# Kernel tuning notes

Measured on AMD Instinct MI355X. Metric: run time of the kernel, lower is better.

Reference implementation:

```python
import jax, jax.numpy as jnp
import numpy as np

# --- model/problem constants (match init_kwargs) ---
B = 1024      # batch
F = 512       # featureSize
H = 1024      # hiddenSize
S = 8         # symmetrySize
BOX = 12      # boxSize
MAXB = 64     # maxBoxes
MAXSY = 64    # maxSyms
MAXS = 16     # max stack depth (pattern uses <= 2)
L = 126


def setup_inputs() -> dict:
    key = jax.random.key(0)
    ks = jax.random.split(key, 9)

    def lin(k, out_d, in_d):
        k1, k2 = jax.random.split(k)
        bound = 1.0 / np.sqrt(in_d)
        W = jax.random.uniform(k1, (out_d, in_d), minval=-bound, maxval=bound, dtype=jnp.float32)
        b = jax.random.uniform(k2, (out_d,), minval=-bound, maxval=bound, dtype=jnp.float32)
        return W, b

    Wd, bd = lin(ks[0], H, F)      # AdjDecoder.decode
    Wl, bl = lin(ks[1], F, H)      # AdjDecoder.left
    Wr, br = lin(ks[2], F, H)      # AdjDecoder.right
    Wsd, bsd = lin(ks[3], H, F)    # SymDecoder.decode
    Wsf, bsf = lin(ks[4], F, H)    # SymDecoder.left
    Wss, bss = lin(ks[5], S, H)    # SymDecoder.right
    Wbox, bbox = lin(ks[6], BOX, F)  # BoxDecoder.decode

    inputStacks = jax.random.normal(ks[7], (B, F), dtype=jnp.float32)

    # Valid stack program, PROCESSING order: [adj, sym, box] * 42.
    # stack depth: 1 ->(1) 2 ->(2) 2 ->(0) 1 ; 42 boxes, 42 syms.
    proc = np.tile(np.array([1, 2, 0], dtype=np.int32), L // 3)
    stored = proc[::-1].copy()  # forward() processes operations in reverse
    operations = jnp.asarray(np.tile(stored[None, None, :], (B, 1, 1)))  # [B,1,L]

    return {"inputStacks": inputStacks, "operations": operations,
            "Wd": Wd, "bd": bd, "Wl": Wl, "bl": bl, "Wr": Wr, "br": br,
            "Wsd": Wsd, "bsd": bsd, "Wsf": Wsf, "bsf": bsf, "Wss": Wss, "bss": bss,
            "Wbox": Wbox, "bbox": bbox}


def _forward(inputStacks, operations, Wd, bd, Wl, bl, Wr, br,
             Wsd, bsd, Wsf, bsf, Wss, bss, Wbox, bbox):
    Bn, Fn = inputStacks.shape
    ops_proc = jnp.flip(operations[:, 0, :], axis=1).T  # [L, B] processing order

    stack = jnp.zeros((Bn, MAXS, Fn), inputStacks.dtype).at[:, 0, :].set(inputStacks)
    sp = jnp.ones((Bn,), jnp.int32)           # stack pointer (size)
    boxbuf = jnp.zeros((Bn, MAXB, Fn), inputStacks.dtype)
    bc = jnp.zeros((Bn,), jnp.int32)
    symbuf = jnp.zeros((Bn, MAXSY, S), inputStacks.dtype)
    sc = jnp.zeros((Bn,), jnp.int32)
    rows = jnp.arange(Bn)

    def step(carry, op):
        stack, sp, boxbuf, bc, symbuf, sc = carry
        top_idx = jnp.clip(sp - 1, 0, MAXS - 1)
        top = stack[rows, top_idx]                      # [B,F]
        # AdjDecoder on every sample (selected by op==1)
        h = jnp.tanh(top @ Wd.T + bd)
        l = jnp.tanh(h @ Wl.T + bl)
        r = jnp.tanh(h @ Wr.T + br)
        # SymDecoder on every sample (selected by op==2)
        hs = jnp.tanh(top @ Wsd.T + bsd)
        f = jnp.tanh(hs @ Wsf.T + bsf)
        s = jnp.tanh(hs @ Wss.T + bss)

        is0 = op == 0
        is1 = op == 1
        is2 = op == 2
        # value replacing the popped top (for op 1 -> left, op 2 -> folded)
        val_top = jnp.where(is1[:, None], l, jnp.where(is2[:, None], f, top))
        pos = jnp.arange(MAXS)[None, :]
        m_top = (pos == top_idx[:, None]) & (~is0)[:, None]
        m_r = (pos == jnp.clip(sp, 0, MAXS - 1)[:, None]) & is1[:, None]
        stack = jnp.where(m_r[..., None], r[:, None, :],
                          jnp.where(m_top[..., None], val_top[:, None, :], stack))
        posb = jnp.arange(MAXB)[None, :]
        mb = (posb == bc[:, None]) & is0[:, None]
        boxbuf = jnp.where(mb[..., None], top[:, None, :], boxbuf)
        poss = jnp.arange(MAXSY)[None, :]
        ms = (poss == sc[:, None]) & is2[:, None]
        symbuf = jnp.where(ms[..., None], s[:, None, :], symbuf)

        sp = sp + jnp.where(is0, -1, jnp.where(is1, 1, 0)).astype(sp.dtype)
        bc = bc + is0.astype(bc.dtype)
        sc = sc + is2.astype(sc.dtype)
        return (stack, sp, boxbuf, bc, symbuf, sc), None

    (stack, sp, boxbuf, bc, symbuf, sc), _ = jax.lax.scan(
        step, (stack, sp, boxbuf, bc, symbuf, sc), ops_proc)

    # boxStacks[i].reverse(); boxDecoder; pad with zeros to maxBoxes
    jb = jnp.arange(MAXB)
    bidx = bc[:, None] - 1 - jb[None, :]          # reversed order
    bvalid = bidx >= 0
    bfeat = jnp.take_along_axis(boxbuf, jnp.clip(bidx, 0, MAXB - 1)[..., None], axis=1)
    boxes = jnp.tanh(bfeat @ Wbox.T + bbox) * bvalid[..., None].astype(bfeat.dtype)

    js = jnp.arange(MAXSY)
    sidx = sc[:, None] - 1 - js[None, :]
    svalid = sidx >= 0
    syms = jnp.take_along_axis(symbuf, jnp.clip(sidx, 0, MAXSY - 1)[..., None], axis=1)
    syms = syms * svalid[..., None].astype(syms.dtype)

    return boxes, syms  # [B, MAXB, BOX], [B, MAXSY, S]


def reference(inputStacks, operations, Wd, bd, Wl, bl, Wr, br,
              Wsd, bsd, Wsf, bsf, Wss, bss, Wbox, bbox):
    return _forward(inputStacks, operations, Wd, bd, Wl, bl, Wr, br,
                    Wsd, bsd, Wsf, bsf, Wss, bss, Wbox, bbox)
```

## Files before the change

kernel.cpp:

```cpp
#include <hip/hip_runtime.h>
#include <stdint.h>

#define B_     1024
#define F_     512
#define H_     1024
#define S_     8
#define BOX_   12
#define MAXB_  64
#define MAXSY_ 64
#define L_     126
#define STK_   3
#define NCYC_  42

typedef unsigned short u16;
typedef unsigned int   u32;
typedef unsigned long long u64;
typedef __attribute__((ext_vector_type(8))) short sh8;
typedef __attribute__((ext_vector_type(4))) int   i4;
typedef __attribute__((ext_vector_type(4))) float f4;

#define MFMA16(a,b,c) __builtin_amdgcn_mfma_f32_16x16x32_bf16((a),(b),(c),0,0,0)

#define XCC_ID_IMM (((32 - 1) << 11) | (0 << 6) | 20)

#define POLL_MAX (1 << 22)

constexpr size_t O_FLAG  = 2048;
constexpr size_t O_GFAIL = 2176;
constexpr size_t O_GXCD  = 2304;
constexpr size_t PL_HF = (size_t)H_ * F_ * 2;
constexpr size_t PL_FH = (size_t)F_ * H_ * 2;
constexpr size_t PL_SS = 16384;
constexpr size_t PL_BX = 16384;
constexpr size_t O_WdHi  = 8192;
constexpr size_t O_WdLo  = O_WdHi  + PL_HF;
constexpr size_t O_WsdHi = O_WdLo  + PL_HF;
constexpr size_t O_WsdLo = O_WsdHi + PL_HF;
constexpr size_t O_WlHi  = O_WsdLo + PL_HF;
constexpr size_t O_WlLo  = O_WlHi  + PL_FH;
constexpr size_t O_WrHi  = O_WlLo  + PL_FH;
constexpr size_t O_WrLo  = O_WrHi  + PL_FH;
constexpr size_t O_WsfHi = O_WrLo  + PL_FH;
constexpr size_t O_WsfLo = O_WsfHi + PL_FH;
constexpr size_t O_WssHi = O_WsfLo + PL_FH;
constexpr size_t O_WssLo = O_WssHi + PL_SS;
constexpr size_t O_WbxHi = O_WssLo + PL_SS;
constexpr size_t O_WbxLo = O_WbxHi + PL_BX;
constexpr size_t SZ_STK  = (size_t)B_ * STK_ * F_ * 2;
constexpr size_t O_SHi   = O_WbxLo + PL_BX;
constexpr size_t O_SLo   = O_SHi   + SZ_STK;
constexpr size_t SZ_H    = (size_t)B_ * H_ * 2;
constexpr size_t O_HAHi  = O_SLo   + SZ_STK;
constexpr size_t O_HALo  = O_HAHi  + SZ_H;
constexpr size_t O_HSHi  = O_HALo  + SZ_H;
constexpr size_t O_HSLo  = O_HSHi  + SZ_H;
constexpr size_t SZ_FB   = (size_t)B_ * 512 * 2;
constexpr size_t O_FB0Hi = O_HSLo  + SZ_H;
constexpr size_t O_FB0Lo = O_FB0Hi + SZ_FB;
constexpr size_t O_FB1Hi = O_FB0Lo + SZ_FB;
constexpr size_t O_FB1Lo = O_FB1Hi + SZ_FB;
constexpr size_t WS_NEED = O_FB1Lo + SZ_FB;

__device__ __forceinline__ float bf2float(u16 h) {
    union { u32 u; float f; } v; v.u = ((u32)h) << 16; return v.f;
}
__device__ __forceinline__ u16 bfhi_of(float f) {
    union { float f; u32 u; } v; v.f = f;
    u32 u = v.u;
    return (u16)((u + 0x7fffu + ((u >> 16) & 1u)) >> 16);
}
__device__ __forceinline__ void split2(float x, u16& hi, u16& lo) {
    hi = bfhi_of(x);
    lo = bfhi_of(x - bf2float(hi));
}

template<bool DC>
__device__ __forceinline__ void cst(u16* p, u16 v) {
    if (DC) asm volatile("global_store_short %0, %1, off sc0 sc1"
                         :: "v"(p), "v"((u32)v) : "memory");
    else    asm volatile("global_store_short %0, %1, off"
                         :: "v"(p), "v"((u32)v) : "memory");
}
__device__ __forceinline__ void vdrain() {
    asm volatile("s_waitcnt vmcnt(0)" ::: "memory");
}

__device__ __forceinline__ void cld8(i4& d0, i4& d1, i4& d2, i4& d3,
                                     i4& d4, i4& d5, i4& d6, i4& d7,
    const u16* p0, const u16* p1, const u16* p2, const u16* p3,
    const u16* p4, const u16* p5, const u16* p6, const u16* p7)
{
    asm volatile(
        "global_load_dwordx4 %0, %8, off sc0\n\t"
        "global_load_dwordx4 %1, %9, off sc0\n\t"
        "global_load_dwordx4 %2, %10, off sc0\n\t"
        "global_load_dwordx4 %3, %11, off sc0\n\t"
        "global_load_dwordx4 %4, %12, off sc0\n\t"
        "global_load_dwordx4 %5, %13, off sc0\n\t"
        "global_load_dwordx4 %6, %14, off sc0\n\t"
        "global_load_dwordx4 %7, %15, off sc0\n\t"
        "s_waitcnt vmcnt(0)"
        : "=&v"(d0),"=&v"(d1),"=&v"(d2),"=&v"(d3),
          "=&v"(d4),"=&v"(d5),"=&v"(d6),"=&v"(d7)
        : "v"(p0),"v"(p1),"v"(p2),"v"(p3),"v"(p4),"v"(p5),"v"(p6),"v"(p7));
}

__device__ void split_range(const float* __restrict__ s, u16* hi, u16* lo,
                            int n, int t0, int stride) {
    for (int i = t0; i < n; i += stride) {
        float v = s[i];
        u16 h = bfhi_of(v);
        hi[i] = h;
        lo[i] = bfhi_of(v - bf2float(h));
    }
}

__global__ void grass_prep(const float* __restrict__ X, const int* __restrict__ ops,
                           const float* __restrict__ Wd, const float* __restrict__ Wl,
                           const float* __restrict__ Wr, const float* __restrict__ Wsd,
                           const float* __restrict__ Wsf, const float* __restrict__ Wss,
                           const float* __restrict__ Wbox, char* __restrict__ ws)
{
    const int t0 = blockIdx.x * blockDim.x + threadIdx.x;
    const int st = gridDim.x * blockDim.x;
    split_range(Wd,  (u16*)(ws + O_WdHi),  (u16*)(ws + O_WdLo),  H_ * F_, t0, st);
    split_range(Wsd, (u16*)(ws + O_WsdHi), (u16*)(ws + O_WsdLo), H_ * F_, t0, st);
    split_range(Wl,  (u16*)(ws + O_WlHi),  (u16*)(ws + O_WlLo),  F_ * H_, t0, st);
    split_range(Wr,  (u16*)(ws + O_WrHi),  (u16*)(ws + O_WrLo),  F_ * H_, t0, st);
    split_range(Wsf, (u16*)(ws + O_WsfHi), (u16*)(ws + O_WsfLo), F_ * H_, t0, st);
    split_range(Wss, (u16*)(ws + O_WssHi), (u16*)(ws + O_WssLo), S_ * H_, t0, st);
    split_range(Wbox,(u16*)(ws + O_WbxHi), (u16*)(ws + O_WbxLo), BOX_ * F_, t0, st);
    u16* SHi = (u16*)(ws + O_SHi);
    u16* SLo = (u16*)(ws + O_SLo);
    for (int i = t0; i < B_ * F_; i += st) {
        int e = i >> 9, k = i & (F_ - 1);
        float v = X[i];
        u16 h = bfhi_of(v);
        size_t off = (size_t)e * STK_ * F_ + k;
        SHi[off] = h;
        SLo[off] = bfhi_of(v - bf2float(h));
    }
    int* flag = (int*)(ws + O_FLAG);
    for (int i = t0; i < B_ * L_; i += st) {
        int t = i % L_;
        int tm = t % 3;
        int expect = (tm == 0) ? 0 : ((tm == 1) ? 2 : 1);
        if (ops[i] != expect) {
            __hip_atomic_store(flag, 1, __ATOMIC_RELAXED, __HIP_MEMORY_SCOPE_AGENT);
            break;
        }
    }
}

__device__ __forceinline__ void gbar(int* bar, int target) {
    vdrain();
    __syncthreads();
    if (threadIdx.x == 0) {
        __hip_atomic_fetch_add(bar, 1, __ATOMIC_RELAXED, __HIP_MEMORY_SCOPE_AGENT);
        while (__hip_atomic_load(bar, __ATOMIC_RELAXED, __HIP_MEMORY_SCOPE_AGENT) < target)
            __builtin_amdgcn_s_sleep(2);
    }
    __syncthreads();
}
__device__ __forceinline__ void gbarT(int* bar, int target) {
    vdrain();
    __syncthreads();
    if (threadIdx.x == 0) {
        __hip_atomic_fetch_add(bar, 1, __ATOMIC_RELAXED, __HIP_MEMORY_SCOPE_AGENT);
        for (int it = 0; it < POLL_MAX; ++it) {
            if (__hip_atomic_load(bar, __ATOMIC_RELAXED, __HIP_MEMORY_SCOPE_AGENT) >= target) break;
            __builtin_amdgcn_s_sleep(2);
        }
    }
    __syncthreads();
}
__device__ __forceinline__ void gwaitT(int* ctr, int target) {
    if (threadIdx.x == 0) {
        for (int it = 0; it < POLL_MAX; ++it) {
            if (__hip_atomic_load(ctr, __ATOMIC_RELAXED, __HIP_MEMORY_SCOPE_AGENT) >= target) break;
            __builtin_amdgcn_s_sleep(2);
        }
    }
    __syncthreads();
}

__device__ __forceinline__ void stage256(u16* __restrict__ lds,
    const u16* __restrict__ AHi, const u16* __restrict__ ALo,
    const int* __restrict__ aOff, int kbase, int tid)
{
    const int wv = tid >> 6, lane = tid & 63;
    const int rsub = lane >> 5;
    const int c8 = (lane & 31) * 8;
    int off[8];
#pragma unroll
    for (int i = 0; i < 8; ++i) off[i] = aOff[i * 8 + wv * 2 + rsub] + kbase + c8;
    const int sw = ((wv * 2 + rsub) & 7) << 3;
    i4 d0,d1,d2,d3,d4,d5,d6,d7;
    cld8(d0,d1,d2,d3,d4,d5,d6,d7,
         AHi+off[0], AHi+off[1], AHi+off[2], AHi+off[3],
         AHi+off[4], AHi+off[5], AHi+off[6], AHi+off[7]);
#define STO(ii, dv, base) { const int m = (ii) * 8 + wv * 2 + rsub; \
                            *(i4*)((base) + m * 256 + (c8 ^ sw)) = dv; }
    STO(0,d0,lds) STO(1,d1,lds) STO(2,d2,lds) STO(3,d3,lds)
    STO(4,d4,lds) STO(5,d5,lds) STO(6,d6,lds) STO(7,d7,lds)
    cld8(d0,d1,d2,d3,d4,d5,d6,d7,
         ALo+off[0], ALo+off[1], ALo+off[2], ALo+off[3],
         ALo+off[4], ALo+off[5], ALo+off[6], ALo+off[7]);
    u16* ldsLo = lds + 64 * 256;
    STO(0,d0,ldsLo) STO(1,d1,ldsLo) STO(2,d2,ldsLo) STO(3,d3,ldsLo)
    STO(4,d4,ldsLo) STO(5,d5,ldsLo) STO(6,d6,ldsLo) STO(7,d7,ldsLo)
#undef STO
}

__device__ __forceinline__ void stageA_dc(u16* __restrict__ lds,
    const u16* __restrict__ AHi, const u16* __restrict__ ALo,
    const int* __restrict__ aOff, int kbase, int tid)
{
    const int wv = tid >> 6, lane = tid & 63;
    const int kk = kbase + lane * 8;
    int off[16];
#pragma unroll
    for (int i = 0; i < 16; ++i) off[i] = aOff[i * 4 + wv] + kk;
    u64 v[64];
#pragma unroll
    for (int i = 0; i < 16; ++i) {
        const u64* s = (const u64*)(AHi + off[i]);
        v[2 * i]     = __hip_atomic_load(s,     __ATOMIC_RELAXED, __HIP_MEMORY_SCOPE_AGENT);
        v[2 * i + 1] = __hip_atomic_load(s + 1, __ATOMIC_RELAXED, __HIP_MEMORY_SCOPE_AGENT);
    }
#pragma unroll
    for (int i = 0; i < 16; ++i) {
        const u64* s = (const u64*)(ALo + off[i]);
        v[32 + 2 * i] = __hip_atomic_load(s,     __ATOMIC_RELAXED, __HIP_MEMORY_SCOPE_AGENT);
        v[33 + 2 * i] = __hip_atomic_load(s + 1, __ATOMIC_RELAXED, __HIP_MEMORY_SCOPE_AGENT);
    }
#pragma unroll
    for (int i = 0; i < 16; ++i) {
        const int m = i * 4 + wv;
        u16* d = lds + m * 512 + ((lane * 8) ^ ((m & 7) << 3));
        ((u64*)d)[0] = v[2 * i];
        ((u64*)d)[1] = v[2 * i + 1];
        u64* d2 = (u64*)(d + 32768);
        d2[0] = v[32 + 2 * i];
        d2[1] = v[33 + 2 * i];
    }
}

template<int CW>
__device__ __forceinline__ void kloop64(const u16* __restrict__ lds,
    const u16* __restrict__ WHi, const u16* __restrict__ WLo,
    int nRow0, int Kw, int kofs, f4 c[2][2], int lane, int wv4)
{
    const int quad = lane >> 4, mr = lane & 15;
    const int mh = wv4 & 1, nh = (wv4 >> 1) & 1;
    const int m0 = (mh * 2) * 16 + mr, m1 = m0 + 16;
    const int n0 = nRow0 + (nh * 2) * 16 + mr, n1 = n0 + 16;
    const u16* b0h = WHi + (size_t)n0 * Kw + kofs;
    const u16* b1h = WHi + (size_t)n1 * Kw + kofs;
    const u16* b0l = WLo + (size_t)n0 * Kw + kofs;
    const u16* b1l = WLo + (size_t)n1 * Kw + kofs;
    const int sw = (m0 & 7) << 3;
    const u16* A0h = lds + m0 * CW;
    const u16* A1h = lds + m1 * CW;
#pragma unroll 2
    for (int kb = 0; kb < CW; kb += 64) {
        const int k0 = kb + quad * 8, k1 = k0 + 32;
        const int x0 = k0 ^ sw, x1 = k1 ^ sw;
        sh8 B0H0 = *(const sh8*)(b0h + k0), B1H0 = *(const sh8*)(b1h + k0);
        sh8 B0L0 = *(const sh8*)(b0l + k0), B1L0 = *(const sh8*)(b1l + k0);
        sh8 B0H1 = *(const sh8*)(b0h + k1), B1H1 = *(const sh8*)(b1h + k1);
        sh8 B0L1 = *(const sh8*)(b0l + k1), B1L1 = *(const sh8*)(b1l + k1);
        sh8 A0H0 = *(const sh8*)(A0h + x0);
        sh8 A1H0 = *(const sh8*)(A1h + x0);
        sh8 A0L0 = *(const sh8*)(A0h + 64 * CW + x0);
        sh8 A1L0 = *(const sh8*)(A1h + 64 * CW + x0);
        sh8 A0H1 = *(const sh8*)(A0h + x1);
        sh8 A1H1 = *(const sh8*)(A1h + x1);
        sh8 A0L1 = *(const sh8*)(A0h + 64 * CW + x1);
        sh8 A1L1 = *(const sh8*)(A1h + 64 * CW + x1);
        c[0][0]=MFMA16(A0H0,B0H0,c[0][0]); c[0][1]=MFMA16(A0H0,B1H0,c[0][1]);
        c[1][0]=MFMA16(A1H0,B0H0,c[1][0]); c[1][1]=MFMA16(A1H0,B1H0,c[1][1]);
        c[0][0]=MFMA16(A0H0,B0L0,c[0][0]); c[0][1]=MFMA16(A0H0,B1L0,c[0][1]);
        c[1][0]=MFMA16(A1H0,B0L0,c[1][0]); c[1][1]=MFMA16(A1H0,B1L0,c[1][1]);
        c[0][0]=MFMA16(A0L0,B0H0,c[0][0]); c[0][1]=MFMA16(A0L0,B1H0,c[0][1]);
        c[1][0]=MFMA16(A1L0,B0H0,c[1][0]); c[1][1]=MFMA16(A1L0,B1H0,c[1][1]);
        c[0][0]=MFMA16(A0H1,B0H1,c[0][0]); c[0][1]=MFMA16(A0H1,B1H1,c[0][1]);
        c[1][0]=MFMA16(A1H1,B0H1,c[1][0]); c[1][1]=MFMA16(A1H1,B1H1,c[1][1]);
        c[0][0]=MFMA16(A0H1,B0L1,c[0][0]); c[0][1]=MFMA16(A0H1,B1L1,c[0][1]);
        c[1][0]=MFMA16(A1H1,B0L1,c[1][0]); c[1][1]=MFMA16(A1H1,B1L1,c[1][1]);
        c[0][0]=MFMA16(A0L1,B0H1,c[0][0]); c[0][1]=MFMA16(A0L1,B1H1,c[0][1]);
        c[1][0]=MFMA16(A1L1,B0H1,c[1][0]); c[1][1]=MFMA16(A1L1,B1H1,c[1][1]);
    }
}

template<int CW>
__device__ __forceinline__ void kloop16(const u16* __restrict__ lds,
    const u16* __restrict__ WHi, const u16* __restrict__ WLo,
    int nValid, int Kw, int kofs, f4& c, int lane, int wv)
{
    const int quad = lane >> 4, mr = lane & 15;
    const int m = wv * 16 + mr;
    const int sm = (m & 7) << 3;
    const u16* Am = lds + m * CW;
    const bool nb = (mr < nValid);
    const u16* bh = WHi + (size_t)mr * Kw + kofs;
    const u16* bl = WLo + (size_t)mr * Kw + kofs;
#pragma unroll 2
    for (int kb = 0; kb < CW; kb += 64) {
        const int k0 = kb + quad * 8, k1 = k0 + 32;
        const int x0 = k0 ^ sm, x1 = k1 ^ sm;
        sh8 bH0 = {0,0,0,0,0,0,0,0}, bL0 = {0,0,0,0,0,0,0,0};
        sh8 bH1 = {0,0,0,0,0,0,0,0}, bL1 = {0,0,0,0,0,0,0,0};
        if (nb) {
            bH0 = *(const sh8*)(bh + k0); bL0 = *(const sh8*)(bl + k0);
            bH1 = *(const sh8*)(bh + k1); bL1 = *(const sh8*)(bl + k1);
        }
        sh8 aH0 = *(const sh8*)(Am + x0);
        sh8 aL0 = *(const sh8*)(Am + 64 * CW + x0);
        sh8 aH1 = *(const sh8*)(Am + x1);
        sh8 aL1 = *(const sh8*)(Am + 64 * CW + x1);
        c = MFMA16(aH0, bH0, c);
        c = MFMA16(aH0, bL0, c);
        c = MFMA16(aL0, bH0, c);
        c = MFMA16(aH1, bH1, c);
        c = MFMA16(aH1, bL1, c);
        c = MFMA16(aL1, bH1, c);
    }
}

__device__ __forceinline__ void zacc(f4 c[2][2]) {
    f4 z = {0.f, 0.f, 0.f, 0.f};
    c[0][0] = z; c[0][1] = z; c[1][0] = z; c[1][1] = z;
}

__device__ __forceinline__ void gemmK(u16* __restrict__ Ab,
    const u16* __restrict__ AHi, const u16* __restrict__ ALo, const int* __restrict__ aOff,
    const u16* __restrict__ WHi, const u16* __restrict__ WLo, int nRow0, int Kw,
    f4 c[2][2], int tid, int lane, int wv)
{
    zacc(c);
    for (int h = 0; h < Kw; h += 512) {
        __syncthreads();
        stageA_dc(Ab, AHi, ALo, aOff, h, tid);
        __syncthreads();
        kloop64<512>(Ab, WHi, WLo, nRow0, Kw, h, c, lane, wv);
    }
}
__device__ __forceinline__ void gemmK16(u16* __restrict__ Ab,
    const u16* __restrict__ AHi, const u16* __restrict__ ALo, const int* __restrict__ aOff,
    const u16* __restrict__ WHi, const u16* __restrict__ WLo, int nValid, int Kw,
    f4& c, int tid, int lane, int wv)
{
    f4 z = {0.f, 0.f, 0.f, 0.f};
    c = z;
    for (int h = 0; h < Kw; h += 512) {
        __syncthreads();
        stageA_dc(Ab, AHi, ALo, aOff, h, tid);
        __syncthreads();
        kloop16<512>(Ab, WHi, WLo, nValid, Kw, h, c, lane, wv);
    }
}

__device__ __forceinline__ void pipe_gemm64(u16* __restrict__ Ab,
    const u16* __restrict__ AHi, const u16* __restrict__ ALo, const int* __restrict__ aOff,
    const u16* __restrict__ WHi, const u16* __restrict__ WLo, int col0, int Kw,
    f4 c[2][2], int tid, int lane, int wv)
{
    zacc(c);
    for (int h = 0; h < Kw; h += 256) {
        __syncthreads();
        stage256(Ab, AHi, ALo, aOff, h, tid);
        __syncthreads();
        kloop64<256>(Ab, WHi, WLo, col0, Kw, h, c, lane, wv);
    }
}

template<bool DC>
__device__ __forceinline__ void ep_h(const f4 c[2][2], const float* __restrict__ bias,
                                     int colBase, int e0, u16* DHi, u16* DLo,
                                     int lane, int wv4)
{
    const int quad = lane >> 4, mr = lane & 15;
    const int mh = wv4 & 1, nh = (wv4 >> 1) & 1;
#pragma unroll
    for (int mi = 0; mi < 2; ++mi)
#pragma unroll
    for (int ni = 0; ni < 2; ++ni)
#pragma unroll
    for (int r = 0; r < 4; ++r) {
        int mm = (mh * 2 + mi) * 16 + quad * 4 + r;
        int nn = (nh * 2 + ni) * 16 + mr;
        float v = tanhf(c[mi][ni][r] + bias[colBase + nn]);
        u16 hi, lo; split2(v, hi, lo);
        size_t off = (size_t)(e0 + mm) * H_ + colBase + nn;
        cst<DC>(DHi + off, hi);
        cst<DC>(DLo + off, lo);
    }
}

template<bool DC>
__device__ __forceinline__ void ep_slot(const f4 c[2][2], const float* __restrict__ bias,
                                        int colBase, int slot, int e0,
                                        u16* SHi, u16* SLo, int lane, int wv4)
{
    const int quad = lane >> 4, mr = lane & 15;
    const int mh = wv4 & 1, nh = (wv4 >> 1) & 1;
#pragma unroll
    for (int mi = 0; mi < 2; ++mi)
#pragma unroll
    for (int ni = 0; ni < 2; ++ni)
#pragma unroll
    for (int r = 0; r < 4; ++r) {
        int mm = (mh * 2 + mi) * 16 + quad * 4 + r;
        int nn = (nh * 2 + ni) * 16 + mr;
        float v = tanhf(c[mi][ni][r] + bias[colBase + nn]);
        u16 hi, lo; split2(v, hi, lo);
        size_t off = ((size_t)(e0 + mm) * STK_ + slot) * F_ + colBase + nn;
        cst<DC>(SHi + off, hi);
        cst<DC>(SLo + off, lo);
    }
}

template<bool DC>
__device__ __forceinline__ void ep_fb(const f4 c[2][2], const float* __restrict__ bias,
                                      int colBase, int e0, u16* FHi, u16* FLo,
                                      int lane, int wv4)
{
    const int quad = lane >> 4, mr = lane & 15;
    const int mh = wv4 & 1, nh = (wv4 >> 1) & 1;
#pragma unroll
    for (int mi = 0; mi < 2; ++mi)
#pragma unroll
    for (int ni = 0; ni < 2; ++ni)
#pragma unroll
    for (int r = 0; r < 4; ++r) {
        int mm = (mh * 2 + mi) * 16 + quad * 4 + r;
        int nn = (nh * 2 + ni) * 16 + mr;
        float v = tanhf(c[mi][ni][r] + bias[colBase + nn]);
        u16 hi, lo; split2(v, hi, lo);
        size_t off = (size_t)(e0 + mm) * 512 + colBase + nn;
        cst<DC>(FHi + off, hi);
        cst<DC>(FLo + off, lo);
    }
}

template<bool DC>
__device__ __forceinline__ void ep_stack(const f4 c[2][2], const float* __restrict__ bias,
                                         int colBase, int opSel, bool useRi, int tix, int e0,
                                         const unsigned char* opsL, const int* spA,
                                         u16* SHi, u16* SLo, int lane, int wv)
{
    const int quad = lane >> 4, mr = lane & 15;
    const int mh = wv & 1, nh = (wv >> 1) & 1;
#pragma unroll
    for (int mi = 0; mi < 2; ++mi)
#pragma unroll
    for (int ni = 0; ni < 2; ++ni)
#pragma unroll
    for (int r = 0; r < 4; ++r) {
        int mm = (mh * 2 + mi) * 16 + quad * 4 + r;
        int nn = (nh * 2 + ni) * 16 + mr;
        if (opsL[mm * L_ + tix] != opSel) continue;
        int sp = spA[mm];
        int slot = useRi ? sp : sp - 1;
        slot = slot < 0 ? 0 : (slot > STK_ - 1 ? STK_ - 1 : slot);
        float v = tanhf(c[mi][ni][r] + bias[colBase + nn]);
        u16 hi, lo; split2(v, hi, lo);
        size_t off = ((size_t)(e0 + mm) * STK_ + slot) * F_ + colBase + nn;
        cst<DC>(SHi + off, hi);
        cst<DC>(SLo + off, lo);
    }
}

__device__ __forceinline__ void ep_small(const f4& c, const float* __restrict__ bias,
                                         int nValid, int opSel, int tix, int e0,
                                         const unsigned char* opsL, const int* eCnt, const int* eTot,
                                         float* __restrict__ outBase, int rowStride, int ncols,
                                         int lane, int wv)
{
    const int nn = lane & 15;
    if (nn >= nValid) return;
#pragma unroll
    for (int r = 0; r < 4; ++r) {
        int mm = wv * 16 + (lane >> 4) * 4 + r;
        if (opsL[mm * L_ + tix] != opSel) continue;
        int slot = eTot[mm] - 1 - eCnt[mm];
        if (slot < 0 || slot >= 64) continue;
        float v = tanhf(c[r] + bias[nn]);
        outBase[(size_t)(e0 + mm) * rowStride + slot * ncols + nn] = v;
    }
}

__device__ __forceinline__ void ep_small_u(const f4& c, const float* __restrict__ bias,
                                           int nValid, int slot, int e0,
                                           float* __restrict__ outBase, int rowStride, int ncols,
                                           int lane, int wv)
{
    const int nn = lane & 15;
    if (nn >= nValid) return;
#pragma unroll
    for (int r = 0; r < 4; ++r) {
        int mm = wv * 16 + (lane >> 4) * 4 + r;
        outBase[(size_t)(e0 + mm) * rowStride + slot * ncols + nn] = tanhf(c[r] + bias[nn]);
    }
}

__global__ __launch_bounds__(256, 2) void grass_pipe(
    const float* __restrict__ bd, const float* __restrict__ bl, const float* __restrict__ br,
    const float* __restrict__ bsd, const float* __restrict__ bsf, const float* __restrict__ bss,
    const float* __restrict__ bbox,
    char* __restrict__ ws, float* __restrict__ out)
{
    if (__hip_atomic_load((int*)(ws + O_FLAG), __ATOMIC_RELAXED, __HIP_MEMORY_SCOPE_AGENT))
        return;

    const int tid  = threadIdx.x;
    const int lane = tid & 63, wv = tid >> 6;
    const int j    = blockIdx.x >> 4;
    const int gid  = blockIdx.x & 15;
    const int e0   = gid * 64;

    const u16* WdHi  = (const u16*)(ws + O_WdHi);
    const u16* WdLo  = (const u16*)(ws + O_WdLo);
    const u16* WsdHi = (const u16*)(ws + O_WsdHi);
    const u16* WsdLo = (const u16*)(ws + O_WsdLo);
    const u16* WlHi  = (const u16*)(ws + O_WlHi);
    const u16* WlLo  = (const u16*)(ws + O_WlLo);
    const u16* WrHi  = (const u16*)(ws + O_WrHi);
    const u16* WrLo  = (const u16*)(ws + O_WrLo);
    const u16* WsfHi = (const u16*)(ws + O_WsfHi);
    const u16* WsfLo = (const u16*)(ws + O_WsfLo);
    const u16* WssHi = (const u16*)(ws + O_WssHi);
    const u16* WssLo = (const u16*)(ws + O_WssLo);
    const u16* WbxHi = (const u16*)(ws + O_WbxHi);
    const u16* WbxLo = (const u16*)(ws + O_WbxLo);
    u16* SHi  = (u16*)(ws + O_SHi);
    u16* SLo  = (u16*)(ws + O_SLo);
    u16* HAHi = (u16*)(ws + O_HAHi);
    u16* HALo = (u16*)(ws + O_HALo);
    u16* HSHi = (u16*)(ws + O_HSHi);
    u16* HSLo = (u16*)(ws + O_HSLo);
    u16* FB0Hi = (u16*)(ws + O_FB0Hi);
    u16* FB0Lo = (u16*)(ws + O_FB0Lo);
    u16* FB1Hi = (u16*)(ws + O_FB1Hi);
    u16* FB1Lo = (u16*)(ws + O_FB1Lo);
    int* cbar = (int*)ws + gid * 32;
    int* sbar = cbar + 1;
    int* pbar = cbar + 3;
    int* gx   = (int*)(ws + O_GXCD) + gid * 32;
    int* gf   = (int*)(ws + O_GFAIL) + gid;

    float* outB = out;
    float* outS = out + (size_t)B_ * MAXB_ * BOX_;

    __shared__ __align__(16) u16 Abuf[2 * 64 * 256];
    __shared__ int aS0[64], aR1[64], aR2[64], aHH[64], aFB[64];

    if (tid < 64) {
        aS0[tid] = ((e0 + tid) * STK_ + 0) * F_;
        aR1[tid] = ((e0 + tid) * STK_ + 1) * F_;
        aR2[tid] = ((e0 + tid) * STK_ + 2) * F_;
        aHH[tid] = (e0 + tid) * H_;
        aFB[tid] = (e0 + tid) * 512;
    }

    const int myxcd = (int)(__builtin_amdgcn_s_getreg(XCC_ID_IMM) & 0xf);
    if (tid == 0)
        __hip_atomic_store(gx + j, myxcd, __ATOMIC_RELAXED, __HIP_MEMORY_SCOPE_AGENT);
    gbarT(pbar, 32);
    if (tid < 32) {
        int ox = __hip_atomic_load(gx + tid, __ATOMIC_RELAXED, __HIP_MEMORY_SCOPE_AGENT);
        if (ox != myxcd)
            __hip_atomic_store(gf, 1, __ATOMIC_RELAXED, __HIP_MEMORY_SCOPE_AGENT);
    }
    gbarT(pbar, 64);
    if (__hip_atomic_load(gf, __ATOMIC_RELAXED, __HIP_MEMORY_SCOPE_AGENT))
        return;

    f4 cA[2][2];
    f4 cs;

    if (j < 16) {
        for (int cyc = 0; cyc < NCYC_; ++cyc) {
            pipe_gemm64(Abuf, SHi, SLo, aS0, WdHi, WdLo, j * 64, F_, cA, tid, lane, wv);
            ep_h<false>(cA, bd, j * 64, e0, HAHi, HALo, lane, wv);
            gbarT(cbar, 16 * (2 * cyc + 1));
            if (j < 8) {
                pipe_gemm64(Abuf, HAHi, HALo, aHH, WlHi, WlLo, j * 64, H_, cA, tid, lane, wv);
                ep_slot<false>(cA, bl, j * 64, 0, e0, SHi, SLo, lane, wv);
            } else {
                const int rs = 1 + (cyc & 1);
                pipe_gemm64(Abuf, HAHi, HALo, aHH, WrHi, WrLo, (j - 8) * 64, H_, cA, tid, lane, wv);
                if (cyc >= 2) gwaitT(sbar, 16 * (2 * (cyc - 2) + 1));
                ep_slot<false>(cA, br, (j - 8) * 64, rs, e0, SHi, SLo, lane, wv);
            }
            gbarT(cbar, 16 * (2 * cyc + 2));
        }
    } else {
        const int role = j - 16;
        for (int cyc = 0; cyc < NCYC_; ++cyc) {
            gwaitT(cbar, 16 * (2 * cyc + 2));
            const int* aR = (cyc & 1) ? aR2 : aR1;
            pipe_gemm64(Abuf, SHi, SLo, aR, WsdHi, WsdLo, role * 64, F_, cA, tid, lane, wv);
            ep_h<false>(cA, bsd, role * 64, e0, HSHi, HSLo, lane, wv);
            gbarT(sbar, 16 * (2 * cyc + 1));
            if (role < 8) {
                u16* FH = (cyc & 1) ? FB1Hi : FB0Hi;
                u16* FL = (cyc & 1) ? FB1Lo : FB0Lo;
                pipe_gemm64(Abuf, HSHi, HSLo, aHH, WsfHi, WsfLo, role * 64, H_, cA, tid, lane, wv);
                ep_fb<false>(cA, bsf, role * 64, e0, FH, FL, lane, wv);
            } else if (role == 8) {
                f4 z = {0.f, 0.f, 0.f, 0.f}; cs = z;
                for (int h = 0; h < H_; h += 256) {
                    __syncthreads();
                    stage256(Abuf, HSHi, HSLo, aHH, h, tid);
                    __syncthreads();
                    kloop16<256>(Abuf, WssHi, WssLo, S_, H_, h, cs, lane, wv);
                }
                ep_small_u(cs, bss, S_, NCYC_ - 1 - cyc, e0, outS, MAXSY_ * S_, S_, lane, wv);
            } else if (role == 9 && cyc >= 1) {
                const u16* FH = ((cyc - 1) & 1) ? FB1Hi : FB0Hi;
                const u16* FL = ((cyc - 1) & 1) ? FB1Lo : FB0Lo;
                f4 z = {0.f, 0.f, 0.f, 0.f}; cs = z;
                for (int h = 0; h < 512; h += 256) {
                    __syncthreads();
                    stage256(Abuf, FH, FL, aFB, h, tid);
                    __syncthreads();
                    kloop16<256>(Abuf, WbxHi, WbxLo, BOX_, 512, h, cs, lane, wv);
                }
                ep_small_u(cs, bbox, BOX_, NCYC_ - (cyc - 1) - 1, e0, outB, MAXB_ * BOX_, BOX_, lane, wv);
            }
            gbarT(sbar, 16 * (2 * cyc + 2));
        }
        if (role == 9) {
            const u16* FH = ((NCYC_ - 1) & 1) ? FB1Hi : FB0Hi;
            const u16* FL = ((NCYC_ - 1) & 1) ? FB1Lo : FB0Lo;
            f4 z = {0.f, 0.f, 0.f, 0.f}; cs = z;
            for (int h = 0; h < 512; h += 256) {
                __syncthreads();
                stage256(Abuf, FH, FL, aFB, h, tid);
                __syncthreads();
                kloop16<256>(Abuf, WbxHi, WbxLo, BOX_, 512, h, cs, lane, wv);
            }
            ep_small_u(cs, bbox, BOX_, 0, e0, outB, MAXB_ * BOX_, BOX_, lane, wv);
        }
    }
}

__global__ __launch_bounds__(256, 2) void grass_legacy(
    const int* __restrict__ ops,
    const float* __restrict__ bd, const float* __restrict__ bl, const float* __restrict__ br,
    const float* __restrict__ bsd, const float* __restrict__ bsf, const float* __restrict__ bss,
    const float* __restrict__ bbox,
    char* __restrict__ ws, float* __restrict__ out)
{
    const int tid  = threadIdx.x;
    const int lane = tid & 63, wv = tid >> 6;
    const int gid  = blockIdx.x >> 4;
    const int j    = blockIdx.x & 15;
    const int e0   = gid * 64;

    {
        int nonuni = __hip_atomic_load((int*)(ws + O_FLAG), __ATOMIC_RELAXED, __HIP_MEMORY_SCOPE_AGENT);
        int gfl = __hip_atomic_load((int*)(ws + O_GFAIL) + gid, __ATOMIC_RELAXED, __HIP_MEMORY_SCOPE_AGENT);
        if (!nonuni && !gfl) return;
    }

    const u16* WdHi  = (const u16*)(ws + O_WdHi);
    const u16* WdLo  = (const u16*)(ws + O_WdLo);
    const u16* WsdHi = (const u16*)(ws + O_WsdHi);
    const u16* WsdLo = (const u16*)(ws + O_WsdLo);
    const u16* WlHi  = (const u16*)(ws + O_WlHi);
    const u16* WlLo  = (const u16*)(ws + O_WlLo);
    const u16* WrHi  = (const u16*)(ws + O_WrHi);
    const u16* WrLo  = (const u16*)(ws + O_WrLo);
    const u16* WsfHi = (const u16*)(ws + O_WsfHi);
    const u16* WsfLo = (const u16*)(ws + O_WsfLo);
    const u16* WssHi = (const u16*)(ws + O_WssHi);
    const u16* WssLo = (const u16*)(ws + O_WssLo);
    const u16* WbxHi = (const u16*)(ws + O_WbxHi);
    const u16* WbxLo = (const u16*)(ws + O_WbxLo);
    u16* SHi  = (u16*)(ws + O_SHi);
    u16* SLo  = (u16*)(ws + O_SLo);
    u16* HAHi = (u16*)(ws + O_HAHi);
    u16* HALo = (u16*)(ws + O_HALo);
    u16* HSHi = (u16*)(ws + O_HSHi);
    u16* HSLo = (u16*)(ws + O_HSLo);
    int* bar = (int*)ws + gid * 32 + 2;

    float* outB = out;
    float* outS = out + (size_t)B_ * MAXB_ * BOX_;

    __shared__ __align__(16) u16 Abuf[2 * 64 * 512];
    __shared__ unsigned char opsL[64 * L_];
    __shared__ int spA[64], beA[64], seA[64], beF[64], seF[64];
    __shared__ int aStk[64], aHH[64];
    __shared__ int sInfo[2];

    for (int idx = tid; idx < 64 * L_; idx += 256) {
        int e = idx / L_, t = idx - e * L_;
        opsL[idx] = (unsigned char)ops[(size_t)(e0 + e) * L_ + t];
    }
    __syncthreads();
    if (tid < 64) {
        spA[tid] = 1; beA[tid] = 0; seA[tid] = 0;
        int cb = 0, cs2 = 0;
        for (int t = 0; t < L_; ++t) {
            int o = opsL[tid * L_ + t];
            cb += (o == 0); cs2 += (o == 2);
        }
        beF[tid] = cb; seF[tid] = cs2;
        aHH[tid]  = (e0 + tid) * H_;
        aStk[tid] = ((e0 + tid) * STK_ + 0) * F_;
    }
    __syncthreads();

    int epoch = 0;
    f4 c[2][2];
    f4 cs;

    for (int step = 0; step < L_; ++step) {
        const int tix = L_ - 1 - step;
        if (wv == 0) {
            int o  = opsL[lane * L_ + tix];
            int sp = spA[lane];
            unsigned long long bo = __ballot(o  == opsL[0 * L_ + tix]);
            unsigned long long bs = __ballot(sp == spA[0]);
            if (lane == 0) {
                sInfo[0] = o;
                sInfo[1] = (bo == ~0ull && bs == ~0ull) ? 1 : 0;
            }
        }
        __syncthreads();
        const int opU = sInfo[0], uni = sInfo[1];

        if (uni) {
            if (opU == 1) {
                gemmK(Abuf, SHi, SLo, aStk, WdHi, WdLo, j * 64, F_, c, tid, lane, wv);
                ep_h<true>(c, bd, j * 64, e0, HAHi, HALo, lane, wv);
                ++epoch; gbar(bar, 16 * epoch);
                {
                    const u16* W2H = (j < 8) ? WlHi : WrHi;
                    const u16* W2L = (j < 8) ? WlLo : WrLo;
                    const float* b2 = (j < 8) ? bl : br;
                    gemmK(Abuf, HAHi, HALo, aHH, W2H, W2L, (j & 7) * 64, H_, c, tid, lane, wv);
                    ep_stack<true>(c, b2, (j & 7) * 64, 1, j >= 8, tix, e0, opsL, spA, SHi, SLo, lane, wv);
                }
                ++epoch; gbar(bar, 16 * epoch);
            } else if (opU == 2) {
                gemmK(Abuf, SHi, SLo, aStk, WsdHi, WsdLo, j * 64, F_, c, tid, lane, wv);
                ep_h<true>(c, bsd, j * 64, e0, HAHi, HALo, lane, wv);
                ++epoch; gbar(bar, 16 * epoch);
                if (j < 8) {
                    gemmK(Abuf, HAHi, HALo, aHH, WsfHi, WsfLo, j * 64, H_, c, tid, lane, wv);
                    ep_stack<true>(c, bsf, j * 64, 2, false, tix, e0, opsL, spA, SHi, SLo, lane, wv);
                } else if (j == 8) {
                    gemmK16(Abuf, HAHi, HALo, aHH, WssHi, WssLo, S_, H_, cs, tid, lane, wv);
                    ep_small(cs, bss, S_, 2, tix, e0, opsL, seA, seF, outS, MAXSY_ * S_, S_, lane, wv);
                }
                ++epoch; gbar(bar, 16 * epoch);
            } else {
                if (j == 0) {
                    gemmK16(Abuf, SHi, SLo, aStk, WbxHi, WbxLo, BOX_, F_, cs, tid, lane, wv);
                    ep_small(cs, bbox, BOX_, 0, tix, e0, opsL, beA, beF, outB, MAXB_ * BOX_, BOX_, lane, wv);
                }
            }
        } else {
            gemmK(Abuf, SHi, SLo, aStk, WdHi, WdLo, j * 64, F_, c, tid, lane, wv);
            ep_h<true>(c, bd, j * 64, e0, HAHi, HALo, lane, wv);
            gemmK(Abuf, SHi, SLo, aStk, WsdHi, WsdLo, j * 64, F_, c, tid, lane, wv);
            ep_h<true>(c, bsd, j * 64, e0, HSHi, HSLo, lane, wv);
            if (j == 0) {
                gemmK16(Abuf, SHi, SLo, aStk, WbxHi, WbxLo, BOX_, F_, cs, tid, lane, wv);
                ep_small(cs, bbox, BOX_, 0, tix, e0, opsL, beA, beF, outB, MAXB_ * BOX_, BOX_, lane, wv);
            }
            ++epoch; gbar(bar, 16 * epoch);
            if (j < 8) {
                gemmK(Abuf, HAHi, HALo, aHH, WlHi, WlLo, j * 64, H_, c, tid, lane, wv);
                ep_stack<true>(c, bl, j * 64, 1, false, tix, e0, opsL, spA, SHi, SLo, lane, wv);
                gemmK(Abuf, HSHi, HSLo, aHH, WsfHi, WsfLo, j * 64, H_, c, tid, lane, wv);
                ep_stack<true>(c, bsf, j * 64, 2, false, tix, e0, opsL, spA, SHi, SLo, lane, wv);
            } else {
                gemmK(Abuf, HAHi, HALo, aHH, WrHi, WrLo, (j - 8) * 64, H_, c, tid, lane, wv);
                ep_stack<true>(c, br, (j & 7) * 64, 1, true, tix, e0, opsL, spA, SHi, SLo, lane, wv);
                if (j == 8) {
                    gemmK16(Abuf, HSHi, HSLo, aHH, WssHi, WssLo, S_, H_, cs, tid, lane, wv);
                    ep_small(cs, bss, S_, 2, tix, e0, opsL, seA, seF, outS, MAXSY_ * S_, S_, lane, wv);
// ... 34 lines not shown
        v=p2[i]; s2+=w0.x*v.x; s2+=w0.y*v.y; s2+=w0.z*v.z; s2+=w0.w*v.w;
        v=p2[i+1]; t2+=w1.x*v.x; t2+=w1.y*v.y; t2+=w1.z*v.z; t2+=w1.w*v.w;
        v=p3[i]; s3+=w0.x*v.x; s3+=w0.y*v.y; s3+=w0.z*v.z; s3+=w0.w*v.w;
        v=p3[i+1]; t3+=w1.x*v.x; t3+=w1.y*v.y; t3+=w1.z*v.z; t3+=w1.w*v.w;
    }
    r0=s0+t0; r1=s1+t1; r2=s2+t2; r3=s3+t3;
}
__device__ __forceinline__ float fdot1(const float* __restrict__ row,
                                       const float* __restrict__ x, int K4)
{
    const float4* r = (const float4*)row; const float4* p = (const float4*)x;
    float s=0.f,t=0.f;
    for (int i = 0; i < K4; i += 2) {
        float4 w0=r[i], v0=p[i], w1=r[i+1], v1=p[i+1];
        s+=w0.x*v0.x; s+=w0.y*v0.y; s+=w0.z*v0.z; s+=w0.w*v0.w;
        t+=w1.x*v1.x; t+=w1.y*v1.y; t+=w1.z*v1.z; t+=w1.w*v1.w;
    }
    return s+t;
}
#define FB_G 4
__global__ __launch_bounds__(1024) void grass_fallback(
    const float* __restrict__ inputStacks, const int* __restrict__ ops,
    const float* __restrict__ Wd, const float* __restrict__ bd,
    const float* __restrict__ Wl, const float* __restrict__ bl,
    const float* __restrict__ Wr, const float* __restrict__ br,
    const float* __restrict__ Wsd, const float* __restrict__ bsd,
    const float* __restrict__ Wsf, const float* __restrict__ bsf,
    const float* __restrict__ Wss, const float* __restrict__ bss,
    const float* __restrict__ Wbox, const float* __restrict__ bbox,
    float* __restrict__ out)
{
    __shared__ float stk[FB_G][STK_][F_];
    __shared__ float hh[FB_G][H_];
    __shared__ float boxtmp[FB_G][MAXB_][BOX_];
    __shared__ float symtmp[FB_G][MAXSY_][S_];
    const int t = threadIdx.x, b0 = blockIdx.x * FB_G;
    for (int idx = t; idx < FB_G*F_; idx += 1024) {
        int g = idx >> 9, k = idx & (F_-1);
        stk[g][0][k] = inputStacks[(size_t)(b0+g)*F_ + k];
    }
    for (int idx = t; idx < FB_G*H_; idx += 1024) hh[idx>>10][idx&(H_-1)] = 0.f;
    int sp[FB_G], bc[FB_G], sc[FB_G];
#pragma unroll
    for (int g = 0; g < FB_G; ++g) { sp[g]=1; bc[g]=0; sc[g]=0; }
    __syncthreads();
    for (int step = 0; step < L_; ++step) {
        int op[FB_G], ti[FB_G], ri[FB_G]; bool a1=false,a2=false,a0=false;
#pragma unroll
        for (int g = 0; g < FB_G; ++g) {
            op[g] = ops[(size_t)(b0+g)*L_ + (L_-1-step)];
            int tt = sp[g]-1; tt = tt<0?0:(tt>STK_-1?STK_-1:tt); ti[g]=tt;
            int rr = sp[g]; ri[g] = rr>STK_-1?STK_-1:rr;
            a1 |= (op[g]==1); a2 |= (op[g]==2); a0 |= (op[g]==0);
        }
        const float *x0=stk[0][ti[0]], *x1=stk[1][ti[1]], *x2=stk[2][ti[2]], *x3=stk[3][ti[3]];
        if (a1) {
            float r0,r1,r2,r3; fdot4(Wd+(size_t)t*F_, x0,x1,x2,x3, F_/4, r0,r1,r2,r3);
            float bb = bd[t];
            if (op[0]==1) hh[0][t]=tanhf(r0+bb); if (op[1]==1) hh[1][t]=tanhf(r1+bb);
            if (op[2]==1) hh[2][t]=tanhf(r2+bb); if (op[3]==1) hh[3][t]=tanhf(r3+bb);
        }
        if (a2) {
            float r0,r1,r2,r3; fdot4(Wsd+(size_t)t*F_, x0,x1,x2,x3, F_/4, r0,r1,r2,r3);
            float bb = bsd[t];
            if (op[0]==2) hh[0][t]=tanhf(r0+bb); if (op[1]==2) hh[1][t]=tanhf(r1+bb);
            if (op[2]==2) hh[2][t]=tanhf(r2+bb); if (op[3]==2) hh[3][t]=tanhf(r3+bb);
        }
        if (a0 && t < FB_G*BOX_) {
            int g = t / BOX_, cc = t - g*BOX_;
            if (op[g]==0) {
                float acc = fdot1(Wbox+(size_t)cc*F_, stk[g][ti[g]], F_/4);
                boxtmp[g][bc[g]][cc] = tanhf(acc + bbox[cc]);
            }
        }
        __syncthreads();
        if (a1) {
            if (t < F_) {
                float r0,r1,r2,r3; fdot4(Wl+(size_t)t*H_, hh[0],hh[1],hh[2],hh[3], H_/4, r0,r1,r2,r3);
                float bb = bl[t];
                if (op[0]==1) stk[0][ti[0]][t]=tanhf(r0+bb); if (op[1]==1) stk[1][ti[1]][t]=tanhf(r1+bb);
                if (op[2]==1) stk[2][ti[2]][t]=tanhf(r2+bb); if (op[3]==1) stk[3][ti[3]][t]=tanhf(r3+bb);
            } else {
                int m = t - F_;
                float r0,r1,r2,r3; fdot4(Wr+(size_t)m*H_, hh[0],hh[1],hh[2],hh[3], H_/4, r0,r1,r2,r3);
                float bb = br[m];
                if (op[0]==1) stk[0][ri[0]][m]=tanhf(r0+bb); if (op[1]==1) stk[1][ri[1]][m]=tanhf(r1+bb);
                if (op[2]==1) stk[2][ri[2]][m]=tanhf(r2+bb); if (op[3]==1) stk[3][ri[3]][m]=tanhf(r3+bb);
            }
        }
        if (a2) {
            if (t < F_) {
                float r0,r1,r2,r3; fdot4(Wsf+(size_t)t*H_, hh[0],hh[1],hh[2],hh[3], H_/4, r0,r1,r2,r3);
                float bb = bsf[t];
                if (op[0]==2) stk[0][ti[0]][t]=tanhf(r0+bb); if (op[1]==2) stk[1][ti[1]][t]=tanhf(r1+bb);
                if (op[2]==2) stk[2][ti[2]][t]=tanhf(r2+bb); if (op[3]==2) stk[3][ti[3]][t]=tanhf(r3+bb);
            } else if (t < F_ + FB_G*S_) {
                int idx = t - F_, g = idx >> 3, cc = idx & 7;
                if (op[g]==2) {
                    float acc = fdot1(Wss+(size_t)cc*H_, hh[g], H_/4);
                    symtmp[g][sc[g]][cc] = tanhf(acc + bss[cc]);
                }
            }
        }
        __syncthreads();
#pragma unroll
        for (int g = 0; g < FB_G; ++g) {
            if (op[g]==1) sp[g]++;
            else if (op[g]==2) sc[g]++;
            else { bc[g]++; sp[g]--; }
        }
    }
#pragma unroll
    for (int g = 0; g < FB_G; ++g) {
        int b = b0 + g;
        float* ob = out + (size_t)b * MAXB_ * BOX_;
        for (int idx = t; idx < MAXB_*BOX_; idx += 1024) {
            int jj = idx / BOX_, cc = idx - jj*BOX_;
            int e = bc[g] - 1 - jj;
            ob[idx] = (e >= 0) ? boxtmp[g][e][cc] : 0.f;
        }
        float* os = out + (size_t)B_*MAXB_*BOX_ + (size_t)b * MAXSY_ * S_;
        for (int idx = t; idx < MAXSY_*S_; idx += 1024) {
            int jj = idx >> 3, cc = idx & 7;
            int e = sc[g] - 1 - jj;
            os[idx] = (e >= 0) ? symtmp[g][e][cc] : 0.f;
        }
    }
}

extern "C" void kernel_launch(void* const* d_in, const int* in_sizes, int n_in,
                              void* d_out, int out_size, void* d_ws, size_t ws_size,
                              hipStream_t stream) {
    (void)in_sizes; (void)n_in;
    const float* X    = (const float*)d_in[0];
    const int*   ops  = (const int*)d_in[1];
    const float* Wd   = (const float*)d_in[2];  const float* bd   = (const float*)d_in[3];
    const float* Wl   = (const float*)d_in[4];  const float* bl   = (const float*)d_in[5];
    const float* Wr   = (const float*)d_in[6];  const float* br   = (const float*)d_in[7];
    const float* Wsd  = (const float*)d_in[8];  const float* bsd  = (const float*)d_in[9];
    const float* Wsf  = (const float*)d_in[10]; const float* bsf  = (const float*)d_in[11];
    const float* Wss  = (const float*)d_in[12]; const float* bss  = (const float*)d_in[13];
    const float* Wbox = (const float*)d_in[14]; const float* bbox = (const float*)d_in[15];
    float* out = (float*)d_out;

    if (ws_size < WS_NEED) {
        grass_fallback<<<dim3(B_/FB_G), dim3(1024), 0, stream>>>(
            X, ops, Wd, bd, Wl, bl, Wr, br, Wsd, bsd, Wsf, bsf, Wss, bss, Wbox, bbox, out);
        return;
    }
    char* ws = (char*)d_ws;
    hipMemsetAsync(d_out, 0, (size_t)out_size * sizeof(float), stream);
    hipMemsetAsync(ws, 0, 8192, stream);
    grass_prep<<<dim3(512), dim3(256), 0, stream>>>(X, ops, Wd, Wl, Wr, Wsd, Wsf, Wss, Wbox, ws);
    grass_pipe<<<dim3(512), dim3(256), 0, stream>>>(bd, bl, br, bsd, bsf, bss, bbox, ws, out);
    grass_legacy<<<dim3(256), dim3(256), 0, stream>>>(ops, bd, bl, br, bsd, bsf, bss, bbox, ws, out);
}
```

Baseline: 2.670 ms.

## Widen pipe GEMM tiles to 128 columns with register-prefetched A staging

Each block in the pipelined kernel now computes 128 output columns instead of 64, so the A tile staged in LDS is reused for two column halves. The grid halves to 256 blocks, with role counts and barrier targets rescaled. Global loads for the next K chunk are issued into registers before the MFMA loop and written to LDS afterward, overlapping load latency with compute. The trade-off is fewer blocks per XCD group, higher register pressure (launch bounds reduced to 1), and longer per-block serial work.

Result: slower. 2.877 ms (+7.8%).

```diff
diff --git a/kernel.cpp b/kernel.cpp
--- a/kernel.cpp
+++ b/kernel.cpp
@@ -105,6 +105,25 @@
         : "v"(p0),"v"(p1),"v"(p2),"v"(p3),"v"(p4),"v"(p5),"v"(p6),"v"(p7));
 }
 
+__device__ __forceinline__ void cld8i(i4& d0, i4& d1, i4& d2, i4& d3,
+                                      i4& d4, i4& d5, i4& d6, i4& d7,
+    const u16* p0, const u16* p1, const u16* p2, const u16* p3,
+    const u16* p4, const u16* p5, const u16* p6, const u16* p7)
+{
+    asm volatile(
+        "global_load_dwordx4 %0, %8, off sc0\n\t"
+        "global_load_dwordx4 %1, %9, off sc0\n\t"
+        "global_load_dwordx4 %2, %10, off sc0\n\t"
+        "global_load_dwordx4 %3, %11, off sc0\n\t"
+        "global_load_dwordx4 %4, %12, off sc0\n\t"
+        "global_load_dwordx4 %5, %13, off sc0\n\t"
+        "global_load_dwordx4 %6, %14, off sc0\n\t"
+        "global_load_dwordx4 %7, %15, off sc0"
+        : "=&v"(d0),"=&v"(d1),"=&v"(d2),"=&v"(d3),
+          "=&v"(d4),"=&v"(d5),"=&v"(d6),"=&v"(d7)
+        : "v"(p0),"v"(p1),"v"(p2),"v"(p3),"v"(p4),"v"(p5),"v"(p6),"v"(p7));
+}
+
 __device__ void split_range(const float* __restrict__ s, u16* hi, u16* lo,
                             int n, int t0, int stride) {
     for (int i = t0; i < n; i += stride) {
@@ -182,6 +201,45 @@
         }
     }
     __syncthreads();
+}
+
+__device__ __forceinline__ void stage_issue(
+    i4& a0, i4& a1, i4& a2, i4& a3, i4& a4, i4& a5, i4& a6, i4& a7,
+    i4& b0, i4& b1, i4& b2, i4& b3, i4& b4, i4& b5, i4& b6, i4& b7,
+    const u16* __restrict__ AHi, const u16* __restrict__ ALo,
+    const int* __restrict__ aOff, int kbase, int tid)
+{
+    const int wv = tid >> 6, lane = tid & 63;
+    const int rsub = lane >> 5;
+    const int c8 = (lane & 31) * 8;
+    int off[8];
+#pragma unroll
+    for (int i = 0; i < 8; ++i) off[i] = aOff[i * 8 + wv * 2 + rsub] + kbase + c8;
+    cld8i(a0,a1,a2,a3,a4,a5,a6,a7,
+          AHi+off[0], AHi+off[1], AHi+off[2], AHi+off[3],
+          AHi+off[4], AHi+off[5], AHi+off[6], AHi+off[7]);
+    cld8i(b0,b1,b2,b3,b4,b5,b6,b7,
+          ALo+off[0], ALo+off[1], ALo+off[2], ALo+off[3],
+          ALo+off[4], ALo+off[5], ALo+off[6], ALo+off[7]);
+}
+__device__ __forceinline__ void stage_write(
+    i4 a0, i4 a1, i4 a2, i4 a3, i4 a4, i4 a5, i4 a6, i4 a7,
+    i4 b0, i4 b1, i4 b2, i4 b3, i4 b4, i4 b5, i4 b6, i4 b7,
+    u16* __restrict__ lds, int tid)
+{
+    vdrain();
+    const int wv = tid >> 6, lane = tid & 63;
+    const int rsub = lane >> 5;
+    const int c8 = (lane & 31) * 8;
+    const int sw = ((wv * 2 + rsub) & 7) << 3;
+    u16* ldsLo = lds + 64 * 256;
+#define STO(ii, dv, base) { const int m = (ii) * 8 + wv * 2 + rsub; \
+                            *(i4*)((base) + m * 256 + (c8 ^ sw)) = dv; }
+    STO(0,a0,lds) STO(1,a1,lds) STO(2,a2,lds) STO(3,a3,lds)
+    STO(4,a4,lds) STO(5,a5,lds) STO(6,a6,lds) STO(7,a7,lds)
+    STO(0,b0,ldsLo) STO(1,b1,ldsLo) STO(2,b2,ldsLo) STO(3,b3,ldsLo)
+    STO(4,b4,ldsLo) STO(5,b5,ldsLo) STO(6,b6,ldsLo) STO(7,b7,ldsLo)
+#undef STO
 }
 
 __device__ __forceinline__ void stage256(u16* __restrict__ lds,
@@ -361,17 +419,30 @@
     }
 }
 
-__device__ __forceinline__ void pipe_gemm64(u16* __restrict__ Ab,
+__device__ __forceinline__ void pipe_gemm128(u16* __restrict__ Ab,
     const u16* __restrict__ AHi, const u16* __restrict__ ALo, const int* __restrict__ aOff,
     const u16* __restrict__ WHi, const u16* __restrict__ WLo, int col0, int Kw,
-    f4 c[2][2], int tid, int lane, int wv)
-{
-    zacc(c);
+    f4 cA[2][2], f4 cB[2][2], int tid, int lane, int wv)
+{
+    zacc(cA); zacc(cB);
+    i4 s0,s1,s2,s3,s4,s5,s6,s7,s8,s9,s10,s11,s12,s13,s14,s15;
+    stage_issue(s0,s1,s2,s3,s4,s5,s6,s7,s8,s9,s10,s11,s12,s13,s14,s15,
+                AHi, ALo, aOff, 0, tid);
+    __syncthreads();
+    stage_write(s0,s1,s2,s3,s4,s5,s6,s7,s8,s9,s10,s11,s12,s13,s14,s15, Ab, tid);
+    __syncthreads();
     for (int h = 0; h < Kw; h += 256) {
-        __syncthreads();
-        stage256(Ab, AHi, ALo, aOff, h, tid);
-        __syncthreads();
-        kloop64<256>(Ab, WHi, WLo, col0, Kw, h, c, lane, wv);
+        const bool more = (h + 256 < Kw);
+        if (more)
+            stage_issue(s0,s1,s2,s3,s4,s5,s6,s7,s8,s9,s10,s11,s12,s13,s14,s15,
+                        AHi, ALo, aOff, h + 256, tid);
+        kloop64<256>(Ab, WHi, WLo, col0,      Kw, h, cA, lane, wv);
+        kloop64<256>(Ab, WHi, WLo, col0 + 64, Kw, h, cB, lane, wv);
+        if (more) {
+            __syncthreads();
+            stage_write(s0,s1,s2,s3,s4,s5,s6,s7,s8,s9,s10,s11,s12,s13,s14,s15, Ab, tid);
+            __syncthreads();
+        }
     }
 }
 
@@ -505,7 +576,7 @@
     }
 }
 
-__global__ __launch_bounds__(256, 2) void grass_pipe(
+__global__ __launch_bounds__(256, 1) void grass_pipe(
     const float* __restrict__ bd, const float* __restrict__ bl, const float* __restrict__ br,
     const float* __restrict__ bsd, const float* __restrict__ bsf, const float* __restrict__ bss,
     const float* __restrict__ bbox,
@@ -567,49 +638,54 @@
     const int myxcd = (int)(__builtin_amdgcn_s_getreg(XCC_ID_IMM) & 0xf);
     if (tid == 0)
         __hip_atomic_store(gx + j, myxcd, __ATOMIC_RELAXED, __HIP_MEMORY_SCOPE_AGENT);
-    gbarT(pbar, 32);
-    if (tid < 32) {
+    gbarT(pbar, 16);
+    if (tid < 16) {
         int ox = __hip_atomic_load(gx + tid, __ATOMIC_RELAXED, __HIP_MEMORY_SCOPE_AGENT);
         if (ox != myxcd)
             __hip_atomic_store(gf, 1, __ATOMIC_RELAXED, __HIP_MEMORY_SCOPE_AGENT);
     }
-    gbarT(pbar, 64);
+    gbarT(pbar, 32);
     if (__hip_atomic_load(gf, __ATOMIC_RELAXED, __HIP_MEMORY_SCOPE_AGENT))
         return;
 
-    f4 cA[2][2];
+    f4 cA[2][2], cB[2][2];
     f4 cs;
 
-    if (j < 16) {
+    if (j < 8) {
         for (int cyc = 0; cyc < NCYC_; ++cyc) {
-            pipe_gemm64(Abuf, SHi, SLo, aS0, WdHi, WdLo, j * 64, F_, cA, tid, lane, wv);
-            ep_h<false>(cA, bd, j * 64, e0, HAHi, HALo, lane, wv);
-            gbarT(cbar, 16 * (2 * cyc + 1));
-            if (j < 8) {
-                pipe_gemm64(Abuf, HAHi, HALo, aHH, WlHi, WlLo, j * 64, H_, cA, tid, lane, wv);
-                ep_slot<false>(cA, bl, j * 64, 0, e0, SHi, SLo, lane, wv);
+            pipe_gemm128(Abuf, SHi, SLo, aS0, WdHi, WdLo, j * 128, F_, cA, cB, tid, lane, wv);
+            ep_h<false>(cA, bd, j * 128,      e0, HAHi, HALo, lane, wv);
+            ep_h<false>(cB, bd, j * 128 + 64, e0, HAHi, HALo, lane, wv);
+            gbarT(cbar, 8 * (2 * cyc + 1));
+            if (j < 4) {
+                pipe_gemm128(Abuf, HAHi, HALo, aHH, WlHi, WlLo, j * 128, H_, cA, cB, tid, lane, wv);
+                ep_slot<false>(cA, bl, j * 128,      0, e0, SHi, SLo, lane, wv);
+                ep_slot<false>(cB, bl, j * 128 + 64, 0, e0, SHi, SLo, lane, wv);
             } else {
                 const int rs = 1 + (cyc & 1);
-                pipe_gemm64(Abuf, HAHi, HALo, aHH, WrHi, WrLo, (j - 8) * 64, H_, cA, tid, lane, wv);
-                if (cyc >= 2) gwaitT(sbar, 16 * (2 * (cyc - 2) + 1));
-                ep_slot<false>(cA, br, (j - 8) * 64, rs, e0, SHi, SLo, lane, wv);
+                pipe_gemm128(Abuf, HAHi, HALo, aHH, WrHi, WrLo, (j - 4) * 128, H_, cA, cB, tid, lane, wv);
+                if (cyc >= 2) gwaitT(sbar, 8 * (2 * (cyc - 2) + 1));
+                ep_slot<false>(cA, br, (j - 4) * 128,      rs, e0, SHi, SLo, lane, wv);
+                ep_slot<false>(cB, br, (j - 4) * 128 + 64, rs, e0, SHi, SLo, lane, wv);
             }
-            gbarT(cbar, 16 * (2 * cyc + 2));
+            gbarT(cbar, 8 * (2 * cyc + 2));
         }
     } else {
-        const int role = j - 16;
+        const int role = j - 8;
         for (int cyc = 0; cyc < NCYC_; ++cyc) {
-            gwaitT(cbar, 16 * (2 * cyc + 2));
+            gwaitT(cbar, 8 * (2 * cyc + 2));
             const int* aR = (cyc & 1) ? aR2 : aR1;
-            pipe_gemm64(Abuf, SHi, SLo, aR, WsdHi, WsdLo, role * 64, F_, cA, tid, lane, wv);
-            ep_h<false>(cA, bsd, role * 64, e0, HSHi, HSLo, lane, wv);
-            gbarT(sbar, 16 * (2 * cyc + 1));
-            if (role < 8) {
+            pipe_gemm128(Abuf, SHi, SLo, aR, WsdHi, WsdLo, role * 128, F_, cA, cB, tid, lane, wv);
+            ep_h<false>(cA, bsd, role * 128,      e0, HSHi, HSLo, lane, wv);
+            ep_h<false>(cB, bsd, role * 128 + 64, e0, HSHi, HSLo, lane, wv);
+            gbarT(sbar, 8 * (2 * cyc + 1));
+            if (role < 4) {
                 u16* FH = (cyc & 1) ? FB1Hi : FB0Hi;
                 u16* FL = (cyc & 1) ? FB1Lo : FB0Lo;
-                pipe_gemm64(Abuf, HSHi, HSLo, aHH, WsfHi, WsfLo, role * 64, H_, cA, tid, lane, wv);
-                ep_fb<false>(cA, bsf, role * 64, e0, FH, FL, lane, wv);
-            } else if (role == 8) {
+                pipe_gemm128(Abuf, HSHi, HSLo, aHH, WsfHi, WsfLo, role * 128, H_, cA, cB, tid, lane, wv);
+                ep_fb<false>(cA, bsf, role * 128,      e0, FH, FL, lane, wv);
+                ep_fb<false>(cB, bsf, role * 128 + 64, e0, FH, FL, lane, wv);
+            } else if (role == 4) {
                 f4 z = {0.f, 0.f, 0.f, 0.f}; cs = z;
                 for (int h = 0; h < H_; h += 256) {
                     __syncthreads();
@@ -618,7 +694,7 @@
                     kloop16<256>(Abuf, WssHi, WssLo, S_, H_, h, cs, lane, wv);
                 }
                 ep_small_u(cs, bss, S_, NCYC_ - 1 - cyc, e0, outS, MAXSY_ * S_, S_, lane, wv);
-            } else if (role == 9 && cyc >= 1) {
+            } else if (role == 5 && cyc >= 1) {
                 const u16* FH = ((cyc - 1) & 1) ? FB1Hi : FB0Hi;
                 const u16* FL = ((cyc - 1) & 1) ? FB1Lo : FB0Lo;
                 f4 z = {0.f, 0.f, 0.f, 0.f}; cs = z;
@@ -630,9 +706,9 @@
                 }
                 ep_small_u(cs, bbox, BOX_, NCYC_ - (cyc - 1) - 1, e0, outB, MAXB_ * BOX_, BOX_, lane, wv);
             }
-            gbarT(sbar, 16 * (2 * cyc + 2));
-        }
-        if (role == 9) {
+            gbarT(sbar, 8 * (2 * cyc + 2));
+        }
+        if (role == 5) {
             const u16* FH = ((NCYC_ - 1) & 1) ? FB1Hi : FB0Hi;
             const u16* FL = ((NCYC_ - 1) & 1) ? FB1Lo : FB0Lo;
             f4 z = {0.f, 0.f, 0.f, 0.f}; cs = z;
@@ -973,6 +1049,6 @@
     hipMemsetAsync(d_out, 0, (size_t)out_size * sizeof(float), stream);
     hipMemsetAsync(ws, 0, 8192, stream);
     grass_prep<<<dim3(512), dim3(256), 0, stream>>>(X, ops, Wd, Wl, Wr, Wsd, Wsf, Wss, Wbox, ws);
-    grass_pipe<<<dim3(512), dim3(256), 0, stream>>>(bd, bl, br, bsd, bsf, bss, bbox, ws, out);
+    grass_pipe<<<dim3(256), dim3(256), 0, stream>>>(bd, bl, br, bsd, bsf, bss, bbox, ws, out);
     grass_legacy<<<dim3(256), dim3(256), 0, stream>>>(ops, bd, bl, br, bsd, bsf, bss, bbox, ws, out);
 }
```
